# Kernel tuning notes

Hardware: AMD Instinct MI355X
Metric: run time of the kernel (lower is better)

The kernel has to match this reference:

```python
import jax, jax.numpy as jnp
import numpy as np

DIM = 384
INNER = DIM * 4            # expansion_factor=4 -> inner_dim=1536
E = 5                      # num_experts
K = 2                      # num_actives
KS = 31                    # conv kernel size
SQ = DIM // 8              # senet squeeze dim
B, T = 4, 1024


def _p(key, shape, scale=0.02):
    return jax.random.normal(key, shape, dtype=jnp.float32) * scale


def setup_inputs() -> dict:
    key = jax.random.key(0)
    ks = jax.random.split(key, 24)
    return {
        "res": jax.random.normal(ks[0], (B, T, DIM), dtype=jnp.float32),
        # LayerNorm
        "ln_g": jnp.ones((DIM,), jnp.float32),
        "ln_b": jnp.zeros((DIM,), jnp.float32),
        # depthwise Conv1d (groups=dim): kernel [dim, 1, ks]
        "conv_w": _p(ks[1], (DIM, 1, KS)),
        "conv_b": _p(ks[2], (DIM,)),
        # router: Linear(dim,dim) -> SiLU -> Linear(dim,E)
        "rw1": _p(ks[3], (DIM, DIM)), "rb1": jnp.zeros((DIM,), jnp.float32),
        "rw2": _p(ks[4], (DIM, E)),  "rb2": jnp.zeros((E,), jnp.float32),
        # stacked expert weights
        "we1": _p(ks[5], (E, DIM, 2 * INNER)),   "be1": jnp.zeros((E, 2 * INNER), jnp.float32),
        "we2": _p(ks[6], (E, INNER, 2 * INNER)), "be2": jnp.zeros((E, 2 * INNER), jnp.float32),
        "we3": _p(ks[7], (E, INNER, DIM)),       "be3": jnp.zeros((E, DIM), jnp.float32),
        # senet
        "sw1": _p(ks[8], (DIM, SQ)), "sb1": jnp.zeros((SQ,), jnp.float32),
        "sw2": _p(ks[9], (SQ, DIM)), "sb2": jnp.zeros((DIM,), jnp.float32),
        "senet_res": jnp.ones((DIM,), jnp.float32),
    }


def _layernorm(x, g, b, eps=1e-5):
    mu = jnp.mean(x, axis=-1, keepdims=True)
    var = jnp.mean(jnp.square(x - mu), axis=-1, keepdims=True)
    return (x - mu) * jax.lax.rsqrt(var + eps) * g + b


def _swiglu(h):
    a, g = jnp.split(h, 2, axis=-1)
    return a * jax.nn.silu(g)


def _forward(res, ln_g, ln_b, conv_w, conv_b, rw1, rb1, rw2, rb2,
             we1, be1, we2, be2, we3, be3, sw1, sb1, sw2, sb2, senet_res):
    x = _layernorm(res, ln_g, ln_b)                       # [B,T,D]
    # depthwise conv over time (eval mode, no dropout)
    xt = jnp.transpose(x, (0, 2, 1))                      # [B,D,T]
    c = jax.lax.conv_general_dilated(
        xt, conv_w, window_strides=(1,), padding=[(KS // 2, KS // 2)],
        feature_group_count=DIM, dimension_numbers=("NCH", "OIH", "NCH"))
    h = jnp.transpose(c + conv_b[None, :, None], (0, 2, 1))  # [B,T,D]

    # ---- MoE (eval: no routing noise). Dense-equivalent combine: tokens not
    # routed to an expert get softmax weight exactly 0, so weighted sum matches
    # the original gather/scatter_add math. ----
    tok = h.reshape(B * T, DIM)                           # [N,D]
    rv = jax.nn.silu(tok @ rw1 + rb1) @ rw2 + rb2         # [N,E]
    _, top_idx = jax.lax.top_k(rv, K)                     # [N,K]
    n = tok.shape[0]
    mask = jnp.zeros((n, E), bool).at[jnp.arange(n)[:, None], top_idx].set(True)
    w = jax.nn.softmax(jnp.where(mask, rv, -jnp.inf), axis=1)  # [N,E]

    h1 = _swiglu(jnp.einsum("nd,edh->enh", tok, we1) + be1[:, None, :])  # [E,N,INNER]
    h2 = _swiglu(jnp.einsum("enh,ehk->enk", h1, we2) + be2[:, None, :])  # [E,N,INNER]
    eo = jnp.einsum("enh,ehd->end", h2, we3) + be3[:, None, :]           # [E,N,D]
    y = (tok + jnp.einsum("ne,end->nd", w, eo)).reshape(B, T, DIM)

    # senet gate
    pooled = jnp.mean(x * senet_res + y, axis=-2)          # [B,D]
    gate = jax.nn.sigmoid(jax.nn.silu(pooled @ sw1 + sb1) @ sw2 + sb2)
    return res + y * gate[:, None, :]


def reference(res, ln_g, ln_b, conv_w, conv_b, rw1, rb1, rw2, rb2,
              we1, be1, we2, be2, we3, be3, sw1, sb1, sw2, sb2, senet_res):
    return _forward(res, ln_g, ln_b, conv_w, conv_b, rw1, rb1, rw2, rb2,
                    we1, be1, we2, be2, we3, be3, sw1, sb1, sw2, sb2, senet_res)
```

## Files before the change

### kernel.cpp

```cpp
#include <hip/hip_runtime.h>
#include <stdint.h>

#define DIM 384
#define INNER 1536
#define H2X 3072
#define NE 5
#define NB 4
#define NT 1024
#define NN (NB*NT)
#define KSZ 31
#define SQZ 48
#define NASSIGN (NN*2)

typedef float floatx4 __attribute__((ext_vector_type(4)));
typedef __bf16 bf16x8 __attribute__((ext_vector_type(8)));

__device__ __forceinline__ unsigned short f2bs(float f){
  union { float f; uint32_t u; } v; v.f = f;
  uint32_t r = (v.u + 0x7fffu + ((v.u >> 16) & 1u)) >> 16;
  return (unsigned short)r;
}
__device__ __forceinline__ float bs2f(unsigned short s){
  union { uint32_t u; float f; } v; v.u = ((uint32_t)s) << 16; return v.f;
}
__device__ __forceinline__ float fsigmoid(float x){ return 1.f/(1.f+__expf(-x)); }

__device__ __forceinline__ uint32_t pk2_lo(float a, float b, uint32_t old){
  return __builtin_amdgcn_cvt_pk_fp8_f32(a, b, old, false);
}
__device__ __forceinline__ uint32_t pk2_hi(float a, float b, uint32_t old){
  return __builtin_amdgcn_cvt_pk_fp8_f32(a, b, old, true);
}
__device__ __forceinline__ uint8_t f2fp8(float a){
  return (uint8_t)__builtin_amdgcn_cvt_pk_fp8_f32(a, 0.f, 0u, false);
}

__device__ __forceinline__ void gload16(const void* g, void* l){
  __builtin_amdgcn_global_load_lds(
    reinterpret_cast<const __attribute__((address_space(1))) unsigned int*>(
        reinterpret_cast<uintptr_t>(g)),
    reinterpret_cast<__attribute__((address_space(3))) unsigned int*>(
        (unsigned int)reinterpret_cast<uintptr_t>(l)),
    16, 0, 0);
}

__device__ __forceinline__ int prefix_cnt(const int* __restrict__ cnt, int e){
  int base = 0;
  #pragma unroll
  for(int k=0;k<NE;k++) base += (k<e) ? cnt[k] : 0;
  return base;
}

#define WSCALE 8.f

__device__ __forceinline__ void do_tr_bf16(const float* __restrict__ in,
    unsigned short* __restrict__ out, int R, int C, int cx, int cy){
  __shared__ float tile[32][65];
  int c0 = cx*32, r0 = cy*64;
  int tx = threadIdx.x, ty = threadIdx.y;
  #pragma unroll
  for (int i=0;i<8;i++){
    int r = ty + i*8;
    tile[tx][r] = in[(size_t)(r0+r)*C + c0 + tx];
  }
  __syncthreads();
  #pragma unroll
  for (int i=0;i<4;i++){
    int c = ty + i*8;
    uint32_t lo = f2bs(tile[c][2*tx]);
    uint32_t hi = f2bs(tile[c][2*tx+1]);
    *(uint32_t*)&out[(size_t)(c0+c)*R + r0 + 2*tx] = lo | (hi<<16);
  }
}
__device__ __forceinline__ void do_tr_fp8(const float* __restrict__ in,
    uint8_t* __restrict__ out, int R, int C, int cx, int cy){
  __shared__ float tile[32][65];
  int c0 = cx*32, r0 = cy*64;
  int tx = threadIdx.x, ty = threadIdx.y;
  #pragma unroll
  for (int i=0;i<8;i++){
    int r = ty + i*8;
    tile[tx][r] = in[(size_t)(r0+r)*C + c0 + tx];
  }
  __syncthreads();
  #pragma unroll
  for (int i=0;i<4;i++){
    int c = ty + i*8;
    uint32_t v = pk2_lo(tile[c][2*tx]*WSCALE, tile[c][2*tx+1]*WSCALE, 0u);
    *(unsigned short*)&out[(size_t)(c0+c)*R + r0 + 2*tx] = (unsigned short)(v & 0xffffu);
  }
}

#define TR_N1 (96*6*5)
#define TR_N2 (96*24*5)
#define TR_N3 (12*24*5)
#define TR_N4 (12*6)
__global__ __launch_bounds__(256) void tr_all_kernel(
    const float* __restrict__ we1, uint8_t* __restrict__ w1t,
    const float* __restrict__ we2, uint8_t* __restrict__ w2t,
    const float* __restrict__ we3, uint8_t* __restrict__ w3t,
    const float* __restrict__ rw1, unsigned short* __restrict__ rw1t){
  int bid = blockIdx.x;
  if (bid < TR_N1){
    int z = bid/(96*6), rem = bid%(96*6);
    do_tr_fp8(we1 + (size_t)z*384*3072, w1t + (size_t)z*384*3072, 384, 3072, rem%96, rem/96);
  } else if (bid < TR_N1+TR_N2){
    int idx = bid - TR_N1;
    int z = idx/(96*24), rem = idx%(96*24);
    do_tr_fp8(we2 + (size_t)z*1536*3072, w2t + (size_t)z*1536*3072, 1536, 3072, rem%96, rem/96);
  } else if (bid < TR_N1+TR_N2+TR_N3){
    int idx = bid - TR_N1 - TR_N2;
    int z = idx/(12*24), rem = idx%(12*24);
    do_tr_fp8(we3 + (size_t)z*1536*384, w3t + (size_t)z*1536*384, 1536, 384, rem%12, rem/12);
  } else {
    int idx = bid - TR_N1 - TR_N2 - TR_N3;
    do_tr_bf16(rw1, rw1t, 384, 384, idx%12, idx/12);
  }
}

#define CTT 16
__global__ __launch_bounds__(384) void convln_kernel(const float* __restrict__ res,
    const float* __restrict__ ln_g, const float* __restrict__ ln_b,
    const float* __restrict__ cw, const float* __restrict__ cb,
    float* __restrict__ x, unsigned short* __restrict__ tokb, float* __restrict__ y){
  __shared__ float tile[(CTT+30)*DIM];
  int b = blockIdx.y, t0 = blockIdx.x*CTT;
  int tid = threadIdx.x;
  int w = tid>>6, lane = tid&63;
  float gw[6], bw[6];
  #pragma unroll
  for(int i=0;i<6;i++){ gw[i]=ln_g[i*64+lane]; bw[i]=ln_b[i*64+lane]; }
  for(int r=w; r<CTT+30; r+=6){
    int gt = t0 - 15 + r;
    if(gt>=0 && gt<NT){
      const float* rp = res + ((size_t)b*NT+gt)*DIM;
      float v[6]; float s=0.f;
      #pragma unroll
      for(int i=0;i<6;i++){ v[i]=rp[i*64+lane]; s+=v[i]; }
      #pragma unroll
      for(int o=32;o;o>>=1) s += __shfl_down(s,o);
      s = __shfl(s,0);
      float mean = s*(1.f/DIM);
      float q=0.f;
      #pragma unroll
      for(int i=0;i<6;i++){ v[i]-=mean; q+=v[i]*v[i]; }
      #pragma unroll
      for(int o=32;o;o>>=1) q += __shfl_down(q,o);
      q = __shfl(q,0);
      float rstd = rsqrtf(q*(1.f/DIM) + 1e-5f);
      #pragma unroll
      for(int i=0;i<6;i++) tile[r*DIM+i*64+lane] = v[i]*rstd*gw[i]+bw[i];
    } else {
      #pragma unroll
      for(int i=0;i<6;i++) tile[r*DIM+i*64+lane] = 0.f;
    }
  }
  __syncthreads();
  float cwr[KSZ];
  #pragma unroll
  for(int k=0;k<KSZ;k++) cwr[k] = cw[tid*KSZ+k];
  float bias = cb[tid];
  float win[CTT+30];
  #pragma unroll
  for(int r=0;r<CTT+30;r++) win[r] = tile[r*DIM+tid];
  #pragma unroll
  for(int t=0;t<CTT;t++){
    float acc = bias;
    #pragma unroll
    for(int k=0;k<KSZ;k++) acc += win[t+k]*cwr[k];
    size_t o = ((size_t)b*NT + t0 + t)*DIM + tid;
    y[o]=acc; tokb[o]=f2bs(acc);
    x[o]=win[t+15];
  }
}

__global__ __launch_bounds__(256) void router_g1_kernel(const unsigned short* __restrict__ tokb,
    const unsigned short* __restrict__ rw1t, const float* __restrict__ rb1,
    unsigned short* __restrict__ g1, int* __restrict__ cnt){
  int tid = threadIdx.x;
  if(blockIdx.x==0 && blockIdx.y==0 && tid<32) cnt[tid]=0;
  __shared__ alignas(16) unsigned short sA0[128*32];
  __shared__ alignas(16) unsigned short sA1[128*32];
  __shared__ alignas(16) unsigned short sB0[128*32];
  __shared__ alignas(16) unsigned short sB1[128*32];
  int n0 = blockIdx.x*128, m0 = blockIdx.y*128;
  int lane = tid&63, wid = tid>>6, wm = wid&1, wn = wid>>1;
  int l15 = lane&15, quad = lane>>4;
  floatx4 acc[4][4];
  #pragma unroll
  for(int i=0;i<4;i++)
    #pragma unroll
    for(int j=0;j<4;j++) acc[i][j]=(floatx4){0.f,0.f,0.f,0.f};
  int rA = tid>>2, c8 = tid&3;
  const unsigned short* a0p = tokb + (size_t)(m0+rA)*DIM;
  const unsigned short* a1p = tokb + (size_t)(m0+64+rA)*DIM;
  const unsigned short* b0p = rw1t + (size_t)(n0+rA)*DIM;
  const unsigned short* b1p = rw1t + (size_t)(n0+64+rA)*DIM;

  auto stage = [&](int kt, unsigned short* dA, unsigned short* dB){
    gload16(a0p + kt + c8*8, dA + wid*512);
    gload16(a1p + kt + c8*8, dA + 2048 + wid*512);
    gload16(b0p + kt + c8*8, dB + wid*512);
    gload16(b1p + kt + c8*8, dB + 2048 + wid*512);
  };
  auto compute = [&](const unsigned short* cA, const unsigned short* cB){
    bf16x8 af[4], bfr[4];
    #pragma unroll
    for(int mi=0;mi<4;mi++) af[mi] = *(const bf16x8*)&cA[(wm*64+mi*16+l15)*32 + quad*8];
    #pragma unroll
    for(int ni=0;ni<4;ni++) bfr[ni] = *(const bf16x8*)&cB[(wn*64+ni*16+l15)*32 + quad*8];
    #pragma unroll
    for(int mi=0;mi<4;mi++)
      #pragma unroll
      for(int ni=0;ni<4;ni++)
        acc[mi][ni] = __builtin_amdgcn_mfma_f32_16x16x32_bf16(af[mi], bfr[ni], acc[mi][ni],0,0,0);
  };

  stage(0, sA0, sB0);
  __syncthreads();
  for(int kt=0; kt<DIM; kt+=64){
    if (kt+32 < DIM) stage(kt+32, sA1, sB1);
    compute(sA0, sB0);
    __syncthreads();
    if (kt+64 < DIM) stage(kt+64, sA0, sB0);
    compute(sA1, sB1);
    __syncthreads();
  }
  #pragma unroll
  for(int ni=0;ni<4;ni++){
    int col = n0 + wn*64 + ni*16 + l15;
    float bias = rb1[col];
    #pragma unroll
    for(int mi=0;mi<4;mi++){
      int rowb = m0 + wm*64 + mi*16 + quad*4;
      #pragma unroll
      for(int r=0;r<4;r++){
        float v = acc[mi][ni][r] + bias;
        g1[(size_t)(rowb+r)*DIM + col] = f2bs(v*fsigmoid(v));
      }
    }
  }
}

__global__ __launch_bounds__(256) void router2_kernel(const unsigned short* __restrict__ g1,
    const float* __restrict__ rw2, const float* __restrict__ rb2,
    int* __restrict__ ridx, float* __restrict__ rwt, int* __restrict__ cnt){
  __shared__ int hist[8];
  int tid = threadIdx.x;
  int wid = tid>>6, lane = tid&63;
  if(tid<8) hist[tid]=0;
  __syncthreads();
  for(int it=0; it<8; ++it){
    int n = blockIdx.x*32 + wid*8 + it;
    float s[NE]={0.f,0.f,0.f,0.f,0.f};
    #pragma unroll
    for(int i=0;i<6;i++){
      int d = lane + i*64;
      float gv = bs2f(g1[(size_t)n*DIM+d]);
      #pragma unroll
      for(int e=0;e<NE;e++) s[e] += gv * rw2[d*NE+e];
    }
    #pragma unroll
    for(int e=0;e<NE;e++)
      #pragma unroll
      for(int o=32;o;o>>=1) s[e] += __shfl_down(s[e],o);
    if(lane==0){
      float r[NE];
      #pragma unroll
      for(int e=0;e<NE;e++) r[e]=s[e]+rb2[e];
      int e0=0;
      for(int e=1;e<NE;e++) if(r[e]>r[e0]) e0=e;
      int e1=-1;
      for(int e=0;e<NE;e++){ if(e==e0) continue; if(e1<0||r[e]>r[e1]) e1=e; }
      float w0 = 1.f/(1.f+__expf(r[e1]-r[e0]));
      ridx[2*n]=e0; ridx[2*n+1]=e1;
      rwt[2*n]=w0; rwt[2*n+1]=1.f-w0;
      atomicAdd(&hist[e0],1); atomicAdd(&hist[e1],1);
    }
  }
  __syncthreads();
  if(tid<NE) atomicAdd(&cnt[tid], hist[tid]);
}

__global__ __launch_bounds__(256) void fillcompact_kernel(const int* __restrict__ ridx,
    const int* __restrict__ cnt, int* __restrict__ cnt2,
    int* __restrict__ inv, const unsigned short* __restrict__ tokb,
    uint8_t* __restrict__ tokc, float* __restrict__ pooled){
  __shared__ int sSrc[256], sPos[256];
  int tid = threadIdx.x;
  if(blockIdx.x==0){
    for(int i=tid;i<NB*DIM;i+=256) pooled[i]=0.f;
  }
  int i = blockIdx.x*256 + tid;
  int e = ridx[i];
  int base = prefix_cnt(cnt, e);
  int lane = tid&63;
  unsigned long long below = (1ull<<lane)-1ull;
  int pos = 0;
  #pragma unroll
  for(int ex=0; ex<NE; ex++){
    unsigned long long m = __ballot(e==ex);
    if(m){
      int ldr = __ffsll((long long)m)-1;
      int nb = 0;
      if(lane==ldr) nb = atomicAdd(&cnt2[ex], (int)__popcll(m));
      nb = __shfl(nb, ldr);
      if(e==ex) pos = base + nb + (int)__popcll(m & below);
    }
  }
  inv[i] = pos;
  sSrc[tid] = i>>1;
  sPos[tid] = pos;
  __syncthreads();
  int w = tid>>6;
  for(int j=0;j<64;j++){
    int idx = w*64+j;
    int src = sSrc[idx], dst = sPos[idx];
    if(lane<48){
      uint4 sv = ((const uint4*)&tokb[(size_t)src*DIM])[lane];
      float f0=bs2f(sv.x&0xffff)*WSCALE, f1=bs2f(sv.x>>16)*WSCALE;
      float f2=bs2f(sv.y&0xffff)*WSCALE, f3=bs2f(sv.y>>16)*WSCALE;
      float f4=bs2f(sv.z&0xffff)*WSCALE, f5=bs2f(sv.z>>16)*WSCALE;
      float f6=bs2f(sv.w&0xffff)*WSCALE, f7=bs2f(sv.w>>16)*WSCALE;
      uint32_t lo = pk2_hi(f2,f3, pk2_lo(f0,f1,0u));
      uint32_t hi = pk2_hi(f6,f7, pk2_lo(f4,f5,0u));
      uint2 pv; pv.x = lo; pv.y = hi;
      ((uint2*)&tokc[(size_t)dst*DIM])[lane] = pv;
    }
  }
}

template<int KDIM>
__device__ __forceinline__ void gemm_swiglu_impl(
    const uint8_t* __restrict__ A,
    const uint8_t* __restrict__ wt, const float* __restrict__ bias,
    const int* __restrict__ cnt, uint8_t* __restrict__ out,
    float inv_scale, float out_scale){
  int e = blockIdx.z;
  int cn = cnt[e];
  int mtile = blockIdx.y;
  if (mtile*64 >= cn) return;
  int base = prefix_cnt(cnt, e);
  int j0 = blockIdx.x*128;
  int tid=threadIdx.x, lane=tid&63, wid=tid>>6;
  int l15=lane&15, quad=lane>>4;
  __shared__ alignas(16) uint8_t sA0[64*64];
  __shared__ alignas(16) uint8_t sA1[64*64];
  __shared__ alignas(16) uint8_t sBa0[128*64];
  __shared__ alignas(16) uint8_t sBa1[128*64];
  __shared__ alignas(16) uint8_t sBg0[128*64];
  __shared__ alignas(16) uint8_t sBg1[128*64];
  int rA = tid>>2;
  int gb = ((tid&3) ^ ((tid>>3)&3))*16;
  const uint8_t* a0p = A + (size_t)(base + min(mtile*64+rA, cn-1))*KDIM + gb;
  const uint8_t* b0p = wt + ((size_t)e*H2X + j0 + rA)*KDIM + gb;
  const uint8_t* b1p = wt + ((size_t)e*H2X + j0 + 64 + rA)*KDIM + gb;
  const uint8_t* g0p = wt + ((size_t)e*H2X + INNER + j0 + rA)*KDIM + gb;
  const uint8_t* g1p = wt + ((size_t)e*H2X + INNER + j0 + 64 + rA)*KDIM + gb;
  floatx4 aca[4][2], acg[4][2];
  #pragma unroll
  for(int i=0;i<4;i++)
    #pragma unroll
    for(int j=0;j<2;j++){ aca[i][j]=(floatx4){0.f,0.f,0.f,0.f}; acg[i][j]=(floatx4){0.f,0.f,0.f,0.f}; }
  int ldsw = wid*1024;

  auto stage = [&](int kt, uint8_t* dA, uint8_t* dBa, uint8_t* dBg){
    gload16(a0p + kt, dA + ldsw);
    gload16(b0p + kt, dBa + ldsw);
    gload16(b1p + kt, dBa + 4096 + ldsw);
    gload16(g0p + kt, dBg + ldsw);
    gload16(g1p + kt, dBg + 4096 + ldsw);
  };
  auto compute = [&](const uint8_t* cA, const uint8_t* cBa, const uint8_t* cBg){
    #pragma unroll
    for(int s=0;s<2;s++){
      int pq = (((s*4+quad) ^ (l15&6)))*8;
      long af[4], ba[2], bg[2];
      #pragma unroll
      for(int mi=0;mi<4;mi++) af[mi] = *(const long*)&cA[(mi*16+l15)*64 + pq];
      #pragma unroll
      for(int ni=0;ni<2;ni++){
        int col = wid*32 + ni*16 + l15;
        ba[ni] = *(const long*)&cBa[col*64 + pq];
        bg[ni] = *(const long*)&cBg[col*64 + pq];
      }
      #pragma unroll
      for(int mi=0;mi<4;mi++)
        #pragma unroll
        for(int ni=0;ni<2;ni++){
          aca[mi][ni] = __builtin_amdgcn_mfma_f32_16x16x32_fp8_fp8(af[mi], ba[ni], aca[mi][ni],0,0,0);
          acg[mi][ni] = __builtin_amdgcn_mfma_f32_16x16x32_fp8_fp8(af[mi], bg[ni], acg[mi][ni],0,0,0);
        }
    }
  };

  stage(0, sA0, sBa0, sBg0);
  __syncthreads();
  for(int kt=0; kt<KDIM; kt+=128){
    if (kt+64 < KDIM) stage(kt+64, sA1, sBa1, sBg1);
    compute(sA0, sBa0, sBg0);
    __syncthreads();
    if (kt+128 < KDIM) stage(kt+128, sA0, sBa0, sBg0);
    compute(sA1, sBa1, sBg1);
    __syncthreads();
  }

  #pragma unroll
  for(int ni=0;ni<2;ni++){
    int j = j0 + wid*32 + ni*16 + l15;
    float ba_ = bias[e*H2X + j];
    float bg_ = bias[e*H2X + INNER + j];
    #pragma unroll
    for(int mi=0;mi<4;mi++){
      int rl = mi*16 + quad*4;
      #pragma unroll
      for(int r=0;r<4;r++){
        int row = mtile*64 + rl + r;
        if(row < cn){
          float a = aca[mi][ni][r]*inv_scale + ba_;
          float g = acg[mi][ni][r]*inv_scale + bg_;
          out[(size_t)(base+row)*INNER + j] = f2fp8(a*g*fsigmoid(g)*out_scale);
        }
      }
    }
  }
}

__global__ __launch_bounds__(256,3) void gemm_sg1_kernel(
    const uint8_t* __restrict__ A, const uint8_t* __restrict__ wt,
    const float* __restrict__ bias, const int* __restrict__ cnt, uint8_t* __restrict__ out){
  gemm_swiglu_impl<DIM>(A, wt, bias, cnt, out, 1.f/64.f, 64.f);
}
__global__ __launch_bounds__(256,3) void gemm_sg2_kernel(
    const uint8_t* __restrict__ A, const uint8_t* __restrict__ wt,
    const float* __restrict__ bias, const int* __restrict__ cnt, uint8_t* __restrict__ out){
  gemm_swiglu_impl<INNER>(A, wt, bias, cnt, out, 1.f/512.f, 2097152.f);
}

__global__ __launch_bounds__(256,4) void gemm_out_kernel(
    const uint8_t* __restrict__ h2, const uint8_t* __restrict__ w3t,
    const float* __restrict__ be3, const int* __restrict__ cnt, float* __restrict__ eo){
  int e = blockIdx.z;
  int cn = cnt[e];
  int mtile = blockIdx.y;
  if (mtile*64 >= cn) return;
  int base = prefix_cnt(cnt, e);
  int jt = blockIdx.x % 3, kh = blockIdx.x / 3;
  int n0 = jt*128;
  int koff = kh*768;
  float* eos = eo + (size_t)kh*NASSIGN*DIM;
  int tid=threadIdx.x, lane=tid&63, wid=tid>>6;
  int l15=lane&15, quad=lane>>4;
  __shared__ alignas(16) uint8_t sA0[64*64];
  __shared__ alignas(16) uint8_t sA1[64*64];
  __shared__ alignas(16) uint8_t sB0[128*64];
  __shared__ alignas(16) uint8_t sB1[128*64];
  int rA = tid>>2;
  int gb = ((tid&3) ^ ((tid>>3)&3))*16;
  const uint8_t* a0p = h2 + (size_t)(base + min(mtile*64+rA, cn-1))*INNER + koff + gb;
  const uint8_t* b0p = w3t + ((size_t)e*DIM + n0 + rA)*INNER + koff + gb;
  const uint8_t* b1p = w3t + ((size_t)e*DIM + n0 + 64 + rA)*INNER + koff + gb;
  floatx4 acc[4][2];
  #pragma unroll
  for(int i=0;i<4;i++)
    #pragma unroll
    for(int j=0;j<2;j++) acc[i][j]=(floatx4){0.f,0.f,0.f,0.f};
  int ldsw = wid*1024;

  auto stage = [&](int kt, uint8_t* dA, uint8_t* dB){
    gload16(a0p + kt, dA + ldsw);
    gload16(b0p + kt, dB + ldsw);
    gload16(b1p + kt, dB + 4096 + ldsw);
  };
  auto compute = [&](const uint8_t* cA, const uint8_t* cB){
    #pragma unroll
    for(int s=0;s<2;s++){
      int pq = (((s*4+quad) ^ (l15&6)))*8;
      long af[4], bfr[2];
      #pragma unroll
      for(int mi=0;mi<4;mi++) af[mi] = *(const long*)&cA[(mi*16+l15)*64 + pq];
      #pragma unroll
      for(int ni=0;ni<2;ni++){
        int col = wid*32 + ni*16 + l15;
        bfr[ni] = *(const long*)&cB[col*64 + pq];
      }
      #pragma unroll
      for(int mi=0;mi<4;mi++)
        #pragma unroll
        for(int ni=0;ni<2;ni++)
          acc[mi][ni] = __builtin_amdgcn_mfma_f32_16x16x32_fp8_fp8(af[mi], bfr[ni], acc[mi][ni],0,0,0);
    }
  };

  stage(0, sA0, sB0);
  __syncthreads();
  for(int kt=0; kt<768; kt+=128){
    if (kt+64 < 768) stage(kt+64, sA1, sB1);
    compute(sA0, sB0);
    __syncthreads();
    if (kt+128 < 768) stage(kt+128, sA0, sB0);
    compute(sA1, sB1);
    __syncthreads();
  }

  const float OSC = 5.9604644775390625e-8f;
  #pragma unroll
  for(int ni=0;ni<2;ni++){
    int col = n0 + wid*32 + ni*16 + l15;
    float b3 = (kh==0) ? be3[e*DIM + col] : 0.f;
    #pragma unroll
    for(int mi=0;mi<4;mi++){
      int rl = mi*16 + quad*4;
      #pragma unroll
      for(int r=0;r<4;r++){
        int row = mtile*64 + rl + r;
        if(row < cn){
          eos[(size_t)(base+row)*DIM + col] = acc[mi][ni][r]*OSC + b3;
        }
      }
    }
  }
}

__global__ __launch_bounds__(384) void combine_pooled_kernel(const float* __restrict__ eo,
    const int* __restrict__ inv, const float* __restrict__ rwt,
    const float* __restrict__ x, const float* __restrict__ sres,
    float* __restrict__ y, float* __restrict__ pooled){
  int b = blockIdx.y, t0 = blockIdx.x*8;
  int d = threadIdx.x;
  const float* eo1 = eo + (size_t)NASSIGN*DIM;
  float sr = sres[d];
  float acc = 0.f;
  for(int t=0;t<8;t++){
    int n = b*NT + t0 + t;
    int p0 = inv[2*n], p1 = inv[2*n+1];
    float w0 = rwt[2*n], w1 = rwt[2*n+1];
    size_t o = (size_t)n*DIM + d;
    float yv = y[o] + w0*(eo[(size_t)p0*DIM+d] + eo1[(size_t)p0*DIM+d])
                    + w1*(eo[(size_t)p1*DIM+d] + eo1[(size_t)p1*DIM+d]);
    y[o] = yv;
    acc += x[o]*sr + yv;
  }
  atomicAdd(&pooled[b*DIM+d], acc*(1.f/NT));
}

__global__ __launch_bounds__(384) void gatefinal_kernel(const float* __restrict__ pooled,
    const float* __restrict__ sw1, const float* __restrict__ sb1,
    const float* __restrict__ sw2, const float* __restrict__ sb2,
    const float* __restrict__ res, const float* __restrict__ y, float* __restrict__ out){
  int b = blockIdx.y, t0 = blockIdx.x*8;
  int d = threadIdx.x;
  __shared__ float sp[DIM];
  __shared__ float sh[SQZ];
  sp[d] = pooled[b*DIM+d];
  __syncthreads();
  if(d<SQZ){
    float a = sb1[d];
    for(int k=0;k<DIM;k++) a += sp[k]*sw1[k*SQZ+d];
    sh[d] = a*fsigmoid(a);
  }
  __syncthreads();
  float a = sb2[d];
  #pragma unroll
  for(int j=0;j<SQZ;j++) a += sh[j]*sw2[j*DIM+d];
  float g = fsigmoid(a);
  for(int t=0;t<8;t++){
    size_t o = ((size_t)b*NT + t0 + t)*DIM + d;
    out[o] = res[o] + y[o]*g;
  }
}

extern "C" void kernel_launch(void* const* d_in, const int* in_sizes, int n_in,
                              void* d_out, int out_size, void* d_ws, size_t ws_size,
                              hipStream_t stream) {
  (void)in_sizes; (void)n_in; (void)out_size; (void)ws_size;
  const float* res   = (const float*)d_in[0];
  const float* ln_g  = (const float*)d_in[1];
  const float* ln_b  = (const float*)d_in[2];
  const float* conv_w= (const float*)d_in[3];
  const float* conv_b= (const float*)d_in[4];
  const float* rw1   = (const float*)d_in[5];
  const float* rb1   = (const float*)d_in[6];
  const float* rw2   = (const float*)d_in[7];
  const float* rb2   = (const float*)d_in[8];
  const float* we1   = (const float*)d_in[9];
  const float* be1   = (const float*)d_in[10];
  const float* we2   = (const float*)d_in[11];
  const float* be2   = (const float*)d_in[12];
  const float* we3   = (const float*)d_in[13];
  const float* be3   = (const float*)d_in[14];
  const float* sw1   = (const float*)d_in[15];
  const float* sb1   = (const float*)d_in[16];
  const float* sw2   = (const float*)d_in[17];
  const float* sb2   = (const float*)d_in[18];
  const float* sres  = (const float*)d_in[19];
  float* out = (float*)d_out;

  char* ws = (char*)d_ws;
  size_t off = 0;
  auto alloc = [&](size_t bytes)->void*{ void* p = ws + off; off = (off + bytes + 255) & ~(size_t)255; return p; };
  float*          x     = (float*)alloc((size_t)NN*DIM*4);
  float*          y     = (float*)alloc((size_t)NN*DIM*4);
  float*          eo    = (float*)alloc((size_t)2*NASSIGN*DIM*4);
  unsigned short* tokb  = (unsigned short*)alloc((size_t)NN*DIM*2);
  uint8_t*        tokc  = (uint8_t*)alloc((size_t)NASSIGN*DIM);
  unsigned short* g1    = (unsigned short*)alloc((size_t)NN*DIM*2);
  uint8_t*        w1t   = (uint8_t*)alloc((size_t)NE*H2X*DIM);
  uint8_t*        w2t   = (uint8_t*)alloc((size_t)NE*H2X*INNER);
  uint8_t*        w3t   = (uint8_t*)alloc((size_t)NE*DIM*INNER);
  unsigned short* rw1t  = (unsigned short*)alloc((size_t)DIM*DIM*2);
  uint8_t*        h1    = (uint8_t*)alloc((size_t)NASSIGN*INNER);
  uint8_t*        h2b   = (uint8_t*)alloc((size_t)NASSIGN*INNER);
  int*            ridx  = (int*)alloc((size_t)NASSIGN*4);
  float*          rwt   = (float*)alloc((size_t)NASSIGN*4);
  int*            inv   = (int*)alloc((size_t)NASSIGN*4);
  int*            cnt   = (int*)alloc(128);
  int*            cnt2  = cnt + 8;
  float*          pooled= (float*)alloc((size_t)NB*DIM*4);

  tr_all_kernel<<<TR_N1+TR_N2+TR_N3+TR_N4, dim3(32,8), 0, stream>>>(
      we1, w1t, we2, w2t, we3, w3t, rw1, rw1t);
  convln_kernel<<<dim3(NT/CTT, NB), 384, 0, stream>>>(
      res, ln_g, ln_b, conv_w, conv_b, x, tokb, y);
  router_g1_kernel<<<dim3(DIM/128, NN/128), 256, 0, stream>>>(tokb, rw1t, rb1, g1, cnt);
  router2_kernel<<<NN/32, 256, 0, stream>>>(g1, rw2, rb2, ridx, rwt, cnt);
  fillcompact_kernel<<<NASSIGN/256, 256, 0, stream>>>(ridx, cnt, cnt2, inv, tokb, tokc, pooled);

  gemm_sg1_kernel<<<dim3(INNER/128, NN/64, NE), 256, 0, stream>>>(tokc, w1t, be1, cnt, h1);
  gemm_sg2_kernel<<<dim3(INNER/128, NN/64, NE), 256, 0, stream>>>(h1, w2t, be2, cnt, h2b);
  gemm_out_kernel<<<dim3(6, NN/64, NE), 256, 0, stream>>>(h2b, w3t, be3, cnt, eo);
  combine_pooled_kernel<<<dim3(NT/8, NB), 384, 0, stream>>>(
      eo, inv, rwt, x, sres, y, pooled);
  gatefinal_kernel<<<dim3(NT/8, NB), 384, 0, stream>>>(
      pooled, sw1, sb1, sw2, sb2, res, y, out);
}
```

Baseline: 442.7 us.

## Pre-swizzle FP8 expert weights into MFMA fragment layout and load B directly to registers

The weight transpose kernel now writes FP8 expert weights in a 16-column by 32-k tiled layout that matches the MFMA B-fragment order. The swiglu and output GEMMs then read each B fragment straight from global memory into registers, with a coalesced 8-byte load per lane. This removes the LDS staging and the shared-memory reads for B. It relies on L2/global latency being hidden by the double-buffered register prefetch, and it raises VGPR pressure, especially in the swiglu kernel with its gate and value fragments.

```diff
diff --git a/kernel.cpp b/kernel.cpp
--- a/kernel.cpp
+++ b/kernel.cpp
@@ -87,7 +87,11 @@
   for (int i=0;i<4;i++){
     int c = ty + i*8;
     uint32_t v = pk2_lo(tile[c][2*tx]*WSCALE, tile[c][2*tx+1]*WSCALE, 0u);
-    *(unsigned short*)&out[(size_t)(c0+c)*R + r0 + 2*tx] = (unsigned short)(v & 0xffffu);
+    int col = c0 + c;
+    int k = r0 + 2*tx;
+    size_t addr = (size_t)(col>>4)*16*R + ((size_t)(k>>5)<<9)
+                + (size_t)(((col&15) + 16*((k>>3)&3))<<3) + (k&7);
+    *(unsigned short*)&out[addr] = (unsigned short)(v & 0xffffu);
   }
 }
 
@@ -346,62 +350,60 @@
   int l15=lane&15, quad=lane>>4;
   __shared__ alignas(16) uint8_t sA0[64*64];
   __shared__ alignas(16) uint8_t sA1[64*64];
-  __shared__ alignas(16) uint8_t sBa0[128*64];
-  __shared__ alignas(16) uint8_t sBa1[128*64];
-  __shared__ alignas(16) uint8_t sBg0[128*64];
-  __shared__ alignas(16) uint8_t sBg1[128*64];
   int rA = tid>>2;
   int gb = ((tid&3) ^ ((tid>>3)&3))*16;
   const uint8_t* a0p = A + (size_t)(base + min(mtile*64+rA, cn-1))*KDIM + gb;
-  const uint8_t* b0p = wt + ((size_t)e*H2X + j0 + rA)*KDIM + gb;
-  const uint8_t* b1p = wt + ((size_t)e*H2X + j0 + 64 + rA)*KDIM + gb;
-  const uint8_t* g0p = wt + ((size_t)e*H2X + INNER + j0 + rA)*KDIM + gb;
-  const uint8_t* g1p = wt + ((size_t)e*H2X + INNER + j0 + 64 + rA)*KDIM + gb;
+  size_t ebase = (size_t)e*H2X*KDIM;
+  const uint8_t* bvp[2]; const uint8_t* gvp[2];
+  #pragma unroll
+  for(int ni=0;ni<2;ni++){
+    int c16 = j0 + wid*32 + ni*16;
+    bvp[ni] = wt + ebase + (size_t)c16*KDIM + lane*8;
+    gvp[ni] = wt + ebase + (size_t)(INNER + c16)*KDIM + lane*8;
+  }
   floatx4 aca[4][2], acg[4][2];
   #pragma unroll
   for(int i=0;i<4;i++)
     #pragma unroll
     for(int j=0;j<2;j++){ aca[i][j]=(floatx4){0.f,0.f,0.f,0.f}; acg[i][j]=(floatx4){0.f,0.f,0.f,0.f}; }
   int ldsw = wid*1024;
-
-  auto stage = [&](int kt, uint8_t* dA, uint8_t* dBa, uint8_t* dBg){
-    gload16(a0p + kt, dA + ldsw);
-    gload16(b0p + kt, dBa + ldsw);
-    gload16(b1p + kt, dBa + 4096 + ldsw);
-    gload16(g0p + kt, dBg + ldsw);
-    gload16(g1p + kt, dBg + 4096 + ldsw);
+  long bv0[2][2], bg0[2][2], bv1[2][2], bg1[2][2];
+
+  auto stageA = [&](int kt, uint8_t* dA){ gload16(a0p + kt, dA + ldsw); };
+  auto loadB = [&](int kt, long (&v)[2][2], long (&g)[2][2]){
+    #pragma unroll
+    for(int ni=0;ni<2;ni++)
+      #pragma unroll
+      for(int s=0;s<2;s++){
+        v[ni][s] = *(const long*)(bvp[ni] + kt*16 + s*512);
+        g[ni][s] = *(const long*)(gvp[ni] + kt*16 + s*512);
+      }
   };
-  auto compute = [&](const uint8_t* cA, const uint8_t* cBa, const uint8_t* cBg){
+  auto compute = [&](const uint8_t* cA, const long (&v)[2][2], const long (&g)[2][2]){
     #pragma unroll
     for(int s=0;s<2;s++){
       int pq = (((s*4+quad) ^ (l15&6)))*8;
-      long af[4], ba[2], bg[2];
+      long af[4];
       #pragma unroll
       for(int mi=0;mi<4;mi++) af[mi] = *(const long*)&cA[(mi*16+l15)*64 + pq];
-      #pragma unroll
-      for(int ni=0;ni<2;ni++){
-        int col = wid*32 + ni*16 + l15;
-        ba[ni] = *(const long*)&cBa[col*64 + pq];
-        bg[ni] = *(const long*)&cBg[col*64 + pq];
-      }
       #pragma unroll
       for(int mi=0;mi<4;mi++)
         #pragma unroll
         for(int ni=0;ni<2;ni++){
-          aca[mi][ni] = __builtin_amdgcn_mfma_f32_16x16x32_fp8_fp8(af[mi], ba[ni], aca[mi][ni],0,0,0);
-          acg[mi][ni] = __builtin_amdgcn_mfma_f32_16x16x32_fp8_fp8(af[mi], bg[ni], acg[mi][ni],0,0,0);
+          aca[mi][ni] = __builtin_amdgcn_mfma_f32_16x16x32_fp8_fp8(af[mi], v[ni][s], aca[mi][ni],0,0,0);
+          acg[mi][ni] = __builtin_amdgcn_mfma_f32_16x16x32_fp8_fp8(af[mi], g[ni][s], acg[mi][ni],0,0,0);
         }
     }
   };
 
-  stage(0, sA0, sBa0, sBg0);
+  stageA(0, sA0); loadB(0, bv0, bg0);
   __syncthreads();
   for(int kt=0; kt<KDIM; kt+=128){
-    if (kt+64 < KDIM) stage(kt+64, sA1, sBa1, sBg1);
-    compute(sA0, sBa0, sBg0);
+    if (kt+64 < KDIM){ stageA(kt+64, sA1); loadB(kt+64, bv1, bg1); }
+    compute(sA0, bv0, bg0);
     __syncthreads();
-    if (kt+128 < KDIM) stage(kt+128, sA0, sBa0, sBg0);
-    compute(sA1, sBa1, sBg1);
+    if (kt+128 < KDIM){ stageA(kt+128, sA0); loadB(kt+128, bv0, bg0); }
+    compute(sA1, bv1, bg1);
     __syncthreads();
   }
 
@@ -453,53 +455,54 @@
   int l15=lane&15, quad=lane>>4;
   __shared__ alignas(16) uint8_t sA0[64*64];
   __shared__ alignas(16) uint8_t sA1[64*64];
-  __shared__ alignas(16) uint8_t sB0[128*64];
-  __shared__ alignas(16) uint8_t sB1[128*64];
   int rA = tid>>2;
   int gb = ((tid&3) ^ ((tid>>3)&3))*16;
   const uint8_t* a0p = h2 + (size_t)(base + min(mtile*64+rA, cn-1))*INNER + koff + gb;
-  const uint8_t* b0p = w3t + ((size_t)e*DIM + n0 + rA)*INNER + koff + gb;
-  const uint8_t* b1p = w3t + ((size_t)e*DIM + n0 + 64 + rA)*INNER + koff + gb;
+  const uint8_t* bvp[2];
+  #pragma unroll
+  for(int ni=0;ni<2;ni++){
+    int c16 = n0 + wid*32 + ni*16;
+    bvp[ni] = w3t + (size_t)e*DIM*INNER + (size_t)c16*INNER + (size_t)koff*16 + lane*8;
+  }
   floatx4 acc[4][2];
   #pragma unroll
   for(int i=0;i<4;i++)
     #pragma unroll
     for(int j=0;j<2;j++) acc[i][j]=(floatx4){0.f,0.f,0.f,0.f};
   int ldsw = wid*1024;
-
-  auto stage = [&](int kt, uint8_t* dA, uint8_t* dB){
-    gload16(a0p + kt, dA + ldsw);
-    gload16(b0p + kt, dB + ldsw);
-    gload16(b1p + kt, dB + 4096 + ldsw);
+  long bv0[2][2], bv1[2][2];
+
+  auto stageA = [&](int kt, uint8_t* dA){ gload16(a0p + kt, dA + ldsw); };
+  auto loadB = [&](int kt, long (&v)[2][2]){
+    #pragma unroll
+    for(int ni=0;ni<2;ni++)
+      #pragma unroll
+      for(int s=0;s<2;s++)
+        v[ni][s] = *(const long*)(bvp[ni] + kt*16 + s*512);
   };
-  auto compute = [&](const uint8_t* cA, const uint8_t* cB){
+  auto compute = [&](const uint8_t* cA, const long (&v)[2][2]){
     #pragma unroll
     for(int s=0;s<2;s++){
       int pq = (((s*4+quad) ^ (l15&6)))*8;
-      long af[4], bfr[2];
+      long af[4];
       #pragma unroll
       for(int mi=0;mi<4;mi++) af[mi] = *(const long*)&cA[(mi*16+l15)*64 + pq];
-      #pragma unroll
-      for(int ni=0;ni<2;ni++){
-        int col = wid*32 + ni*16 + l15;
-        bfr[ni] = *(const long*)&cB[col*64 + pq];
-      }
       #pragma unroll
       for(int mi=0;mi<4;mi++)
         #pragma unroll
         for(int ni=0;ni<2;ni++)
-          acc[mi][ni] = __builtin_amdgcn_mfma_f32_16x16x32_fp8_fp8(af[mi], bfr[ni], acc[mi][ni],0,0,0);
+          acc[mi][ni] = __builtin_amdgcn_mfma_f32_16x16x32_fp8_fp8(af[mi], v[ni][s], acc[mi][ni],0,0,0);
     }
   };
 
-  stage(0, sA0, sB0);
+  stageA(0, sA0); loadB(0, bv0);
   __syncthreads();
   for(int kt=0; kt<768; kt+=128){
-    if (kt+64 < 768) stage(kt+64, sA1, sB1);
-    compute(sA0, sB0);
+    if (kt+64 < 768){ stageA(kt+64, sA1); loadB(kt+64, bv1); }
+    compute(sA0, bv0);
     __syncthreads();
-    if (kt+128 < 768) stage(kt+128, sA0, sB0);
-    compute(sA1, sB1);
+    if (kt+128 < 768){ stageA(kt+128, sA0); loadB(kt+128, bv0); }
+    compute(sA1, bv1);
     __syncthreads();
   }
 
```

After: 446.1 us. About the same (+0.8%).
